# Kernel tuning notes

Hardware: AMD Instinct MI355X
Metric: run time of the kernel (lower is better)

## Reference

```python
import jax, jax.numpy as jnp
import numpy as np

B, T, N, DIN, HID, ED, K = 64, 12, 1024, 2, 64, 10, 2

def setup_inputs() -> dict:
    key = jax.random.key(0)
    ks = jax.random.split(key, 18)
    g = lambda i, shape, s=0.1: jax.random.normal(ks[i], shape, jnp.float32) * s
    return dict(
        x=g(0, (B, T, N, DIN), 1.0),
        node_embeddings=g(1, (N, ED), 1.0),
        # GCRN cell 0 (dim_in=DIN): gate -> 2*HID, update -> HID
        Wg0=g(2, (ED, K, DIN + HID, 2 * HID)), bg0=g(3, (ED, 2 * HID)),
        Wu0=g(4, (ED, K, DIN + HID, HID)),     bu0=g(5, (ED, HID)),
        # GCRN cell 1 (dim_in=HID)
        Wg1=g(6, (ED, K, 2 * HID, 2 * HID)),   bg1=g(7, (ED, 2 * HID)),
        Wu1=g(8, (ED, K, 2 * HID, HID)),       bu1=g(9, (ED, HID)),
        # RelatinoShipConv: pointwise Linear(input_dim -> rnn_units), torch [out,in]
        Wr=g(10, (HID, DIN)), br=g(11, (HID,)),
        # end_conv1: Linear(HID,HID, bias=False) (num_layers>1 branch)
        W1=g(12, (HID, HID)),
        # self.conv: Conv2d(horizon, horizon, (1, HID+1), bias=False), OIHW
        Wc=g(13, (T, T, 1, HID + 1)),
        # end_conv2: Conv2d(horizon, horizon, (1, HID), bias)
        W2=g(14, (T, T, 1, HID)), b2=g(15, (T,)),
        # end_conv3: Conv2d(horizon, horizon, (1, 2), dilation (1, HID), bias)
        W3=g(16, (T, T, 1, 2)), b3=g(17, (T,)),
    )

def _avwgcn(x, supports, E, Wp, bp):
    # x:[B,N,C], supports:[K,N,N], E:[N,ED] -> [B,N,O]  (AGCRN adaptive graph conv)
    xg = jnp.einsum('knm,bmc->bnkc', supports, x)
    W = jnp.einsum('ne,ekio->nkio', E, Wp)
    b = E @ bp
    return jnp.einsum('bnki,nkio->bno', xg, W) + b

def _cell(xt, h, supports, E, Wg, bg, Wu, bu):
    # GCRN GRU cell
    zr = jax.nn.sigmoid(_avwgcn(jnp.concatenate([xt, h], -1), supports, E, Wg, bg))
    z, r = jnp.split(zr, 2, -1)
    hc = jnp.tanh(_avwgcn(jnp.concatenate([xt, z * h], -1), supports, E, Wu, bu))
    return r * h + (1.0 - r) * hc

def _conv2d(x, w, b=None, rhs_dilation=(1, 1)):
    y = jax.lax.conv_general_dilated(x, w, (1, 1), 'VALID',
        rhs_dilation=rhs_dilation, dimension_numbers=('NCHW', 'OIHW', 'NCHW'))
    return y if b is None else y + b[None, :, None, None]

def _forward(x, E, Wg0, bg0, Wu0, bu0, Wg1, bg1, Wu1, bu1, Wr, br, W1, Wc, W2, b2, W3, b3):
    A = jax.nn.softmax(jax.nn.relu(E @ E.T), axis=1)
    supports = jnp.stack([jnp.eye(N, dtype=x.dtype), A], 0)  # [K,N,N]
    # GCRN encoder: python loop over 2 layers, lax.scan over the 12 timesteps
    cur = x
    for (Wg, bg, Wu, bu) in ((Wg0, bg0, Wu0, bu0), (Wg1, bg1, Wu1, bu1)):
        h0 = jnp.zeros((x.shape[0], N, HID), x.dtype)
        def step(h, xt):
            h = _cell(xt, h, supports, E, Wg, bg, Wu, bu)
            return h, h
        _, hs = jax.lax.scan(step, h0, jnp.swapaxes(cur, 0, 1))
        cur = jnp.swapaxes(hs, 0, 1)  # [B,T,N,HID]
    out = cur @ W1.T  # end_conv1 (Linear, no bias); dropout is identity in eval
    relation = x @ Wr.T + br  # [B,T,N,HID]
    # torch einsum 'btnc,knn->kbcnt' takes the DIAGONAL of supports over n
    rg = jnp.einsum('btnc,knn->kbcnt', relation, supports)
    rg = jnp.transpose(rg, (1, 4, 3, 2, 0)).reshape(x.shape[0], T, N, -1)  # [B,12,N,2*HID]
    rst = _conv2d(rg, Wc)  # [B,12,N,HID]
    out = _conv2d(jnp.concatenate([rst, out], -1), W2, b2)  # [B,12,N,HID+1]
    out = _conv2d(out, W3, b3, rhs_dilation=(1, HID))       # [B,12,N,1]
    return out

def reference(x, node_embeddings, Wg0, bg0, Wu0, bu0, Wg1, bg1, Wu1, bu1, Wr, br, W1, Wc, W2, b2, W3, b3):
    return _forward(x, node_embeddings, Wg0, bg0, Wu0, bu0, Wg1, bg1, Wu1, bu1, Wr, br, W1, Wc, W2, b2, W3, b3)
```

## Files before the change

### kernel.cpp

```cpp
#include <hip/hip_runtime.h>

typedef unsigned short u16;
typedef unsigned int   u32;


__device__ __forceinline__ float bf2f(u16 u){ return __uint_as_float(((u32)u)<<16); }
__device__ __forceinline__ u16 f2bf(float f){
  u32 u = __float_as_uint(f);
  return (u16)((u + 0x7fffu + ((u>>16)&1u)) >> 16);
}

__global__ __launch_bounds__(256) void k_A2(const float* __restrict__ E,
    float* __restrict__ A, float* __restrict__ At, float* __restrict__ diagA)
{
  __shared__ float EL[10][1024];
  __shared__ float row[1024];
  __shared__ float red[4];
  int n = blockIdx.x, tid = threadIdx.x;
  for (int idx=tid; idx<10240; idx+=256)
    EL[idx>>10][idx&1023] = E[(idx&1023)*10 + (idx>>10)];
  __syncthreads();
  float en[10];
#pragma unroll
  for (int e=0;e<10;++e) en[e] = EL[e][n];
  float lmax = -1e30f;
#pragma unroll
  for (int j=0;j<4;++j){
    int m = tid*4 + j;
    float d = 0.f;
#pragma unroll
    for (int e=0;e<10;++e) d = fmaf(en[e], EL[e][m], d);
    d = fmaxf(d, 0.f);
    row[m] = d; lmax = fmaxf(lmax, d);
  }
#pragma unroll
  for (int o=32;o>0;o>>=1) lmax = fmaxf(lmax, __shfl_xor(lmax, o));
  if ((tid&63)==0) red[tid>>6] = lmax;
  __syncthreads();
  float mx = fmaxf(fmaxf(red[0],red[1]), fmaxf(red[2],red[3]));
  __syncthreads();
  float lsum = 0.f;
#pragma unroll
  for (int j=0;j<4;++j){
    int m = tid*4 + j;
    float ex = expf(row[m] - mx);
    row[m] = ex; lsum += ex;
  }
#pragma unroll
  for (int o=32;o>0;o>>=1) lsum += __shfl_xor(lsum, o);
  if ((tid&63)==0) red[tid>>6] = lsum;
  __syncthreads();
  float inv = 1.f/(red[0]+red[1]+red[2]+red[3]);
#pragma unroll
  for (int j=0;j<4;++j){
    int m = tid*4 + j;
    float v = row[m]*inv;
    A[(size_t)n*1024 + m]  = v;
    At[(size_t)m*1024 + n] = v;
    if (m == n) diagA[n] = v;
  }
}

__global__ __launch_bounds__(64) void k_b3eff(
    const float* __restrict__ b2, const float* __restrict__ W3,
    const float* __restrict__ b3, float* __restrict__ b3eff)
{
  int o = threadIdx.x;
  if (o < 12){
    float a = b3[o];
    for (int i=0;i<12;++i)
      a += b2[i] * (W3[(o*12+i)*2] + W3[(o*12+i)*2+1]);
    b3eff[o] = a;
  }
}

__global__ __launch_bounds__(256) void k_Vpre(const float* __restrict__ W1,
    const float* __restrict__ W2, float* __restrict__ V)
{
  int idx = blockIdx.x*256 + threadIdx.x;
  if (idx >= 9216) return;
  int c = idx & 63, r = idx >> 6;
  int j = r % 12, i = r / 12;
  float a = 0.f;
  for (int o=0;o<64;++o)
    a = fmaf(W2[(i*12+j)*64+o], W1[o*64+c], a);
  V[idx] = a;
}

__global__ __launch_bounds__(256) void k_Gpre(const float* __restrict__ Wc,
    const float* __restrict__ W2, u16* __restrict__ G)
{
  int idx = blockIdx.x*256 + threadIdx.x;
  int u = idx & 127, r = idx >> 7;
  int ip = r % 12, i = r / 12;
  float a = 0.f;
  int wlo = u>64 ? u-64 : 0;
  int whi = u<63 ? u : 63;
  for (int j=0;j<12;++j){
    const float* w2r = W2 + (i*12+j)*64;
    const float* wcr = Wc + (j*12+ip)*65;
    for (int w=wlo; w<=whi; ++w)
      a = fmaf(w2r[w], wcr[u-w], a);
  }
  G[idx] = f2bf(a);
}

__global__ __launch_bounds__(256) void gemm7(const float* __restrict__ At,
    const float* __restrict__ X0, float* __restrict__ Y0,
    const float* __restrict__ X1, float* __restrict__ Y1)
{
  const float* X = blockIdx.z ? X1 : X0;
  float*       Y = blockIdx.z ? Y1 : Y0;
  int n0 = blockIdx.x * 128;
  long base = (long)blockIdx.y * 65536;
  __shared__ float Al[32*128];
  __shared__ float Xl[32*64];
  int tid = threadIdx.x;
  int tx = tid & 15, ty = tid >> 4;
  float acc[8][4];
#pragma unroll
  for (int r=0;r<8;++r){ acc[r][0]=0;acc[r][1]=0;acc[r][2]=0;acc[r][3]=0; }

  for (int m0=0; m0<1024; m0+=32){
#pragma unroll
    for (int i=0;i<4;++i){
      int fo = tid + i*256;
      int k = fo >> 5, nl4 = fo & 31;
      float4 v = *(const float4*)(At + (size_t)(m0+k)*1024 + n0 + nl4*4);
      *(float4*)(Al + fo*4) = v;
    }
#pragma unroll
    for (int i=0;i<2;++i){
      int fo = tid + i*256;
      float4 v = *(const float4*)(X + base + (long)m0*64 + fo*4);
      *(float4*)(Xl + fo*4) = v;
    }
    __syncthreads();
#pragma unroll
    for (int kk=0;kk<32;++kk){
      float4 xv = *(const float4*)(Xl + kk*64 + tx*4);
      float4 a0 = *(const float4*)(Al + kk*128 + ty*4);
      float4 a1 = *(const float4*)(Al + kk*128 + 64 + ty*4);
      float av[8] = {a0.x,a0.y,a0.z,a0.w,a1.x,a1.y,a1.z,a1.w};
      float xw[4] = {xv.x,xv.y,xv.z,xv.w};
#pragma unroll
      for (int r=0;r<8;++r)
#pragma unroll
        for (int c=0;c<4;++c) acc[r][c] = fmaf(av[r], xw[c], acc[r][c]);
    }
    __syncthreads();
  }
#pragma unroll
  for (int half=0; half<2; ++half)
#pragma unroll
    for (int i=0;i<4;++i){
      int row = n0 + half*64 + ty*4 + i;
      float4 v; v.x=acc[half*4+i][0]; v.y=acc[half*4+i][1];
      v.z=acc[half*4+i][2]; v.w=acc[half*4+i][3];
      *(float4*)&Y[base + (long)row*64 + tx*4] = v;
    }
}

__global__ __launch_bounds__(256) void gemm2x(const float* __restrict__ A,
    const float* __restrict__ x, float* __restrict__ Y)
{
  __shared__ float As[64][65];
  __shared__ float Xs[64][65];
  int n0 = blockIdx.x*64;
  int q0 = blockIdx.y*64;
  int tid = threadIdx.x, c = tid & 63, rq = tid >> 6;
  float acc[16];
#pragma unroll
  for (int j=0;j<16;++j) acc[j]=0.f;
  for (int m0=0; m0<1024; m0+=64){
#pragma unroll
    for (int j=0;j<16;++j){
      int idx = tid + j*256;
      int r = idx>>6, k = idx&63;
      As[r][k] = A[(size_t)(n0+r)*1024 + m0 + k];
      int qg = q0 + k;
      Xs[r][k] = x[(size_t)(qg>>1)*2048 + (size_t)(m0+r)*2 + (qg&1)];
    }
    __syncthreads();
    for (int k=0;k<64;++k){
      float xv = Xs[k][c];
#pragma unroll
      for (int j=0;j<16;++j) acc[j] = fmaf(As[rq+4*j][k], xv, acc[j]);
    }
    __syncthreads();
  }
#pragma unroll
  for (int j=0;j<16;++j)
    Y[(size_t)(n0+rq+4*j)*1536 + q0 + c] = acc[j];
}

template<int L>
__device__ __forceinline__ void gate_body(
    float* __restrict__ inp, float* __restrict__ Wl, float* __restrict__ En,
    const float* __restrict__ Wg, const float* __restrict__ bgp,
    const float* __restrict__ E,
    const float* __restrict__ xsrc, const float* __restrict__ Axt,
    const float* __restrict__ h, const float* __restrict__ Ah,
    float* __restrict__ zh, float* __restrict__ rb, int t, int first,
    int n, int b0, int tid)
{
  constexpr int IX  = (L==0)?2:64;
  constexpr int KI  = 2*(IX+64);
  constexpr int CH  = (L==0)?44:32;
  constexpr int NCH = KI/CH;
  constexpr int O   = 128;

  if (tid < 10) En[tid] = E[n*10 + tid];
  for (int idx=tid; idx<32*IX; idx+=256){
    int bl = idx/IX, i = idx - bl*IX; int b = b0+bl;
    inp[bl*KI + i] = (L==0)
      ? xsrc[(size_t)((b*12+t)*1024+n)*2 + i]
      : xsrc[((size_t)b<<16) + (size_t)n*64 + i];
  }
  for (int idx=tid; idx<2048; idx+=256){
    int bl = idx>>6, c = idx&63; int b = b0+bl;
    inp[bl*KI + IX + c] = first ? 0.f : h[((size_t)b<<16) + (size_t)n*64 + c];
  }
  for (int idx=tid; idx<32*IX; idx+=256){
    int bl = idx/IX, i = idx - bl*IX; int b = b0+bl;
    inp[bl*KI + IX+64+i] = (L==0)
      ? Axt[(size_t)n*1536 + (size_t)(b*12+t)*2 + i]
      : Axt[((size_t)b<<16) + (size_t)n*64 + i];
  }
  for (int idx=tid; idx<2048; idx+=256){
    int bl = idx>>6, c = idx&63; int b = b0+bl;
    inp[bl*KI + 2*IX+64+c] = first ? 0.f : Ah[((size_t)b<<16) + (size_t)n*64 + c];
  }
  __syncthreads();

  int bg = tid >> 5;
  int og = tid & 31;
  float acc[4][4];
#pragma unroll
  for (int d=0;d<4;++d){
    int o = og*4+d;
    float a = 0.f;
#pragma unroll
    for (int e=0;e<10;++e) a = fmaf(En[e], bgp[e*O+o], a);
#pragma unroll
    for (int bl=0;bl<4;++bl) acc[bl][d] = a;
  }

  for (int ch=0; ch<NCH; ++ch){
    for (int idx=tid; idx<CH*O; idx+=256){
      int i = idx>>7, o = idx&127;
      float a = 0.f;
#pragma unroll
      for (int e=0;e<10;++e)
        a = fmaf(En[e], Wg[((size_t)e*KI + ch*CH + i)*O + o], a);
      Wl[i*O + o] = a;
    }
    __syncthreads();
    float4 xq[4], wq[4];
#pragma unroll
    for (int bl=0;bl<4;++bl) xq[bl] = *(const float4*)&inp[(bg*4+bl)*KI + ch*CH];
#pragma unroll
    for (int ii=0;ii<4;++ii) wq[ii] = *(const float4*)&Wl[ii*O + og*4];
    for (int i=0; i<CH; i+=4){
      int i2 = (i+4<CH) ? i+4 : i;
      float4 xq2[4], wq2[4];
#pragma unroll
      for (int bl=0;bl<4;++bl) xq2[bl] = *(const float4*)&inp[(bg*4+bl)*KI + ch*CH + i2];
#pragma unroll
      for (int ii=0;ii<4;++ii) wq2[ii] = *(const float4*)&Wl[(i2+ii)*O + og*4];
      float xv[4][4], wv[4][4];
#pragma unroll
      for (int bl=0;bl<4;++bl){ xv[bl][0]=xq[bl].x; xv[bl][1]=xq[bl].y; xv[bl][2]=xq[bl].z; xv[bl][3]=xq[bl].w; }
#pragma unroll
      for (int ii=0;ii<4;++ii){ wv[ii][0]=wq[ii].x; wv[ii][1]=wq[ii].y; wv[ii][2]=wq[ii].z; wv[ii][3]=wq[ii].w; }
#pragma unroll
      for (int bl=0;bl<4;++bl)
#pragma unroll
        for (int d=0;d<4;++d)
#pragma unroll
          for (int ii=0;ii<4;++ii)
            acc[bl][d] = fmaf(xv[bl][ii], wv[ii][d], acc[bl][d]);
#pragma unroll
      for (int bl=0;bl<4;++bl) xq[bl]=xq2[bl];
#pragma unroll
      for (int ii=0;ii<4;++ii) wq[ii]=wq2[ii];
    }
    __syncthreads();
  }

#pragma unroll
  for (int bl=0;bl<4;++bl){
    int b = b0 + bg*4 + bl;
    size_t base = ((size_t)b<<16) + (size_t)n*64;
#pragma unroll
    for (int d=0;d<4;++d){
      int o = og*4 + d;
      float s = 1.f/(1.f+__expf(-acc[bl][d]));
      if (o < 64){
        if (!first) zh[base+o] = s * h[base+o];
      } else {
        rb[base+o-64] = s;
      }
    }
  }
}

__global__ __launch_bounds__(256) void k_gateB(int l_z0,
    const float* __restrict__ Wg0, const float* __restrict__ bg0,
    const float* __restrict__ Wg1, const float* __restrict__ bg1,
    const float* __restrict__ E,  const float* __restrict__ x,
    const float* __restrict__ Ax0T,
    const float* __restrict__ h0cur, const float* __restrict__ h1,
    const float* __restrict__ Axt1,  const float* __restrict__ AhZ1,
    float* __restrict__ zh0, float* __restrict__ rb0,
    float* __restrict__ zh1, float* __restrict__ rb1,
    int t0, int first0, int first1)
{
  __shared__ float smem[12288];
  __shared__ float En[10];
  int n = blockIdx.x, b0 = blockIdx.y*32, tid = threadIdx.x;
  int L = blockIdx.z ? 0 : l_z0;
  if (L == 1)
    gate_body<1>(smem, smem + 32*256, En, Wg1, bg1, E,
                 h0cur, Axt1, h1, AhZ1, zh1, rb1, 0, first1, n, b0, tid);
  else
    gate_body<0>(smem, smem + 32*132, En, Wg0, bg0, E,
                 x, Ax0T, h0cur, Axt1, zh0, rb0, t0, first0, n, b0, tid);
}

template<int L>
__device__ __forceinline__ void upd_body(
    float* __restrict__ inp, float* __restrict__ Wl, float* __restrict__ En,
    const float* __restrict__ Wu, const float* __restrict__ bup,
    const float* __restrict__ E,
    const float* __restrict__ xsrc, const float* __restrict__ Axt,
    const float* __restrict__ zh, const float* __restrict__ Azh,
    const float* __restrict__ rb,
    const float* __restrict__ hread, float* __restrict__ hwrite,
    const float* __restrict__ V, float* __restrict__ q1acc,
    int t, int tq, int first, int n, int b0, int tid)
{
  constexpr int IX  = (L==0)?2:64;
  constexpr int KI  = 2*(IX+64);
  constexpr int CH  = (L==0)?44:64;
  constexpr int NCH = KI/CH;
  constexpr int O   = 64;

  if (tid < 10) En[tid] = E[n*10 + tid];
  for (int idx=tid; idx<32*IX; idx+=256){
    int bl = idx/IX, i = idx - bl*IX; int b = b0+bl;
    inp[bl*KI + i] = (L==0)
      ? xsrc[(size_t)((b*12+t)*1024+n)*2 + i]
      : xsrc[((size_t)b<<16) + (size_t)n*64 + i];
  }
  for (int idx=tid; idx<2048; idx+=256){
    int bl = idx>>6, c = idx&63; int b = b0+bl;
    inp[bl*KI + IX + c] = first ? 0.f : zh[((size_t)b<<16) + (size_t)n*64 + c];
  }
  for (int idx=tid; idx<32*IX; idx+=256){
    int bl = idx/IX, i = idx - bl*IX; int b = b0+bl;
    inp[bl*KI + IX+64+i] = (L==0)
      ? Axt[(size_t)n*1536 + (size_t)(b*12+t)*2 + i]
      : Axt[((size_t)b<<16) + (size_t)n*64 + i];
  }
  for (int idx=tid; idx<2048; idx+=256){
    int bl = idx>>6, c = idx&63; int b = b0+bl;
    inp[bl*KI + 2*IX+64+c] = first ? 0.f : Azh[((size_t)b<<16) + (size_t)n*64 + c];
  }
  __syncthreads();

  int bg = tid >> 5;
  int og = tid & 31;
  float acc[4][2];
#pragma unroll
  for (int d=0;d<2;++d){
    int o = og*2+d;
    float a = 0.f;
#pragma unroll
    for (int e=0;e<10;++e) a = fmaf(En[e], bup[e*O+o], a);
#pragma unroll
    for (int bl=0;bl<4;++bl) acc[bl][d] = a;
  }

  for (int ch=0; ch<NCH; ++ch){
    for (int idx=tid; idx<CH*O; idx+=256){
      int i = idx>>6, o = idx&63;
      float a = 0.f;
#pragma unroll
      for (int e=0;e<10;++e)
        a = fmaf(En[e], Wu[((size_t)e*KI + ch*CH + i)*O + o], a);
      Wl[i*O + o] = a;
    }
    __syncthreads();
    float4 xq[4]; float2 wq[4];
#pragma unroll
    for (int bl=0;bl<4;++bl) xq[bl] = *(const float4*)&inp[(bg*4+bl)*KI + ch*CH];
#pragma unroll
    for (int ii=0;ii<4;++ii) wq[ii] = *(const float2*)&Wl[ii*O + og*2];
    for (int i=0; i<CH; i+=4){
      int i2 = (i+4<CH) ? i+4 : i;
      float4 xq2[4]; float2 wq2[4];
#pragma unroll
      for (int bl=0;bl<4;++bl) xq2[bl] = *(const float4*)&inp[(bg*4+bl)*KI + ch*CH + i2];
#pragma unroll
      for (int ii=0;ii<4;++ii) wq2[ii] = *(const float2*)&Wl[(i2+ii)*O + og*2];
      float xv[4][4], wv[4][2];
#pragma unroll
      for (int bl=0;bl<4;++bl){ xv[bl][0]=xq[bl].x; xv[bl][1]=xq[bl].y; xv[bl][2]=xq[bl].z; xv[bl][3]=xq[bl].w; }
#pragma unroll
      for (int ii=0;ii<4;++ii){ wv[ii][0]=wq[ii].x; wv[ii][1]=wq[ii].y; }
#pragma unroll
      for (int bl=0;bl<4;++bl)
#pragma unroll
        for (int d=0;d<2;++d)
#pragma unroll
          for (int ii=0;ii<4;++ii)
            acc[bl][d] = fmaf(xv[bl][ii], wv[ii][d], acc[bl][d]);
#pragma unroll
      for (int bl=0;bl<4;++bl) xq[bl]=xq2[bl];
#pragma unroll
      for (int ii=0;ii<4;++ii) wq[ii]=wq2[ii];
    }
    __syncthreads();
  }

  float* hnL = Wl;
  float* VL  = Wl + 2080;
#pragma unroll
  for (int bl=0;bl<4;++bl){
    int b = b0 + bg*4 + bl;
    size_t base = ((size_t)b<<16) + (size_t)n*64;
#pragma unroll
    for (int d=0;d<2;++d){
      int o = og*2 + d;
      float hc = tanhf(acc[bl][d]);
      float r  = rb[base+o];
      float h0v = first ? 0.f : hread[base+o];
      float hn = r*h0v + (1.f-r)*hc;
      hwrite[base+o] = hn;
      if (L==1) hnL[(bg*4+bl)*65 + o] = hn;
    }
  }
  if (L==1){
    for (int idx=tid; idx<768; idx+=256)
      VL[idx] = V[((idx>>6)*12+tq)*64 + (idx&63)];
    __syncthreads();
    for (int task=tid; task<384; task+=256){
      int bl = task & 31, i = task >> 5;
      const float* hv = hnL + bl*65;
      const float* vv = VL + i*64;
      float s = 0.f;
#pragma unroll 8
      for (int c=0;c<64;++c) s = fmaf(hv[c], vv[c], s);
      size_t qi = (((size_t)(b0+bl)<<10) + n)*12 + i;
      if (first) q1acc[qi] = s; else q1acc[qi] += s;
    }
  }
}

__global__ __launch_bounds__(256) void k_updB(int l_z0,
    const float* __restrict__ Wu0, const float* __restrict__ bu0,
    const float* __restrict__ Wu1, const float* __restrict__ bu1,
    const float* __restrict__ E,  const float* __restrict__ x,
    const float* __restrict__ Ax0T, const float* __restrict__ Axt1,
    const float* __restrict__ h0cur, float* __restrict__ h0new,
    float* __restrict__ h1,
    const float* __restrict__ zh0, const float* __restrict__ Azh0,
    const float* __restrict__ rb0,
    const float* __restrict__ zh1, const float* __restrict__ Azh1,
    const float* __restrict__ rb1,
    const float* __restrict__ V, float* __restrict__ q1acc,
    int t0, int t1, int first0, int first1)
{
  __shared__ float smem[12288];
  __shared__ float En[10];
  int n = blockIdx.x, b0 = blockIdx.y*32, tid = threadIdx.x;
  int L = blockIdx.z ? 0 : l_z0;
  if (L == 1)
    upd_body<1>(smem, smem + 32*256, En, Wu1, bu1, E,
                h0cur, Axt1, zh1, Azh1, rb1, h1, h1, V, q1acc,
                0, t1, first1, n, b0, tid);
  else
    upd_body<0>(smem, smem + 32*132, En, Wu0, bu0, E,
                x, Ax0T, zh0, Azh0, rb0, h0cur, h0new, nullptr, nullptr,
                t0, 0, first0, n, b0, tid);
}

__global__ __launch_bounds__(256) void k_q0G(
    const float* __restrict__ x, const float* __restrict__ diagA,
    const u16* __restrict__ G,
    const float* __restrict__ Wr, const float* __restrict__ br,
    float* __restrict__ q0buf)
{
  int n = blockIdx.x, tid = threadIdx.x;
  __shared__ u16  GL[18432];
  __shared__ float xsL[64][25];
  __shared__ float WrL[64][2];
  __shared__ float brL[64];

  for (int idx=tid; idx<18432; idx+=256) GL[idx] = G[idx];
  for (int idx=tid; idx<1536; idx+=256){
    int b = idx/24, r = idx - b*24;
    xsL[b][r] = x[(size_t)((b*12+(r>>1))*1024+n)*2 + (r&1)];
  }
  if (tid<128) WrL[tid>>1][tid&1] = Wr[tid];
  else if (tid<192) brL[tid-128] = br[tid-128];
  __syncthreads();

  float dA = diagA[n];
  int b = tid & 63, iq = tid >> 6;
  int i0 = iq*3;
  float q0a=0.f, q0b=0.f, q0c=0.f;
  for (int ip=0; ip<12; ++ip){
    float xa = xsL[b][ip*2], xb = xsL[b][ip*2+1];
    const u16* g0r = &GL[((i0+0)*12+ip)*128];
    const u16* g1r = &GL[((i0+1)*12+ip)*128];
    const u16* g2r = &GL[((i0+2)*12+ip)*128];
    for (int c=0;c<64;++c){
      float rel  = fmaf(xa, WrL[c][0], fmaf(xb, WrL[c][1], brL[c]));
      float relD = rel * dA;
      u32 g0 = *(const u32*)&g0r[2*c];
      u32 g1 = *(const u32*)&g1r[2*c];
      u32 g2 = *(const u32*)&g2r[2*c];
      q0a = fmaf(rel, bf2f((u16)g0), fmaf(relD, bf2f((u16)(g0>>16)), q0a));
      q0b = fmaf(rel, bf2f((u16)g1), fmaf(relD, bf2f((u16)(g1>>16)), q0b));
      q0c = fmaf(rel, bf2f((u16)g2), fmaf(relD, bf2f((u16)(g2>>16)), q0c));
    }
  }
  size_t qb = (((size_t)b<<10) + n)*12;
  q0buf[qb+i0]   = q0a;
  q0buf[qb+i0+1] = q0b;
  q0buf[qb+i0+2] = q0c;
}

__global__ __launch_bounds__(256) void k_head2(
    const float* __restrict__ q0buf, const float* __restrict__ q1acc,
    const float* __restrict__ W3, const float* __restrict__ b3eff,
    float* __restrict__ out)
{
  int n = blockIdx.x, tid = threadIdx.x;
  __shared__ float W3L[12][12][2];
  __shared__ float b3eL[12];
  __shared__ float q0L[64][12];
  __shared__ float q1L[64][12];

  if (tid < 12) b3eL[tid] = b3eff[tid];
  for (int idx=tid; idx<288; idx+=256){
    int o = idx/24, r = idx - o*24;
    W3L[o][r>>1][r&1] = W3[idx];
  }
  for (int idx=tid; idx<768; idx+=256){
    int b = idx/12, i = idx - (idx/12)*12;
    size_t base = (((size_t)b<<10) + n)*12 + i;
    q0L[b][i] = q0buf[base];
    q1L[b][i] = q1acc[base];
  }
  __syncthreads();

  for (int idx=tid; idx<768; idx+=256){
    int bb = idx/12, o = idx - (idx/12)*12;
    float a = b3eL[o];
#pragma unroll
    for (int i=0;i<12;++i)
      a += q0L[bb][i]*W3L[o][i][0] + q1L[bb][i]*W3L[o][i][1];
    out[(size_t)(bb*12+o)*1024 + n] = a;
  }
}

extern "C" void kernel_launch(void* const* d_in, const int* in_sizes, int n_in,
                              void* d_out, int out_size, void* d_ws, size_t ws_size,
                              hipStream_t stream)
{
  const float* x   = (const float*)d_in[0];
  const float* E   = (const float*)d_in[1];
  const float* Wg0 = (const float*)d_in[2];
  const float* bg0 = (const float*)d_in[3];
  const float* Wu0 = (const float*)d_in[4];
  const float* bu0 = (const float*)d_in[5];
  const float* Wg1 = (const float*)d_in[6];
  const float* bg1 = (const float*)d_in[7];
  const float* Wu1 = (const float*)d_in[8];
  const float* bu1 = (const float*)d_in[9];
  const float* Wr  = (const float*)d_in[10];
  const float* br  = (const float*)d_in[11];
  const float* W1  = (const float*)d_in[12];
  const float* Wc  = (const float*)d_in[13];
  const float* W2  = (const float*)d_in[14];
  const float* b2  = (const float*)d_in[15];
  const float* W3  = (const float*)d_in[16];
  const float* b3  = (const float*)d_in[17];

  char* ws = (char*)d_ws;
  size_t off = 0;
  auto alloc = [&](size_t bytes)->void*{
    void* p = ws + off; off += (bytes + 255) & ~(size_t)255; return p;
  };
  float* A     = (float*)alloc(1024ull*1024*4);
  float* At    = (float*)alloc(1024ull*1024*4);
  float* diagA = (float*)alloc(1024*4);
  float* Ax0T  = (float*)alloc(1024ull*1536*4);
  float* Axt1  = (float*)alloc(64ull*65536*4);
  float* AhZ1  = (float*)alloc(64ull*65536*4);
  float* Azh0  = (float*)alloc(64ull*65536*4);
  float* Azh1  = (float*)alloc(64ull*65536*4);
  float* zh0   = (float*)alloc(64ull*65536*4);
  float* zh1   = (float*)alloc(64ull*65536*4);
  float* rb0   = (float*)alloc(64ull*65536*4);
  float* rb1   = (float*)alloc(64ull*65536*4);
  float* h0a   = (float*)alloc(64ull*65536*4);
  float* h0b   = (float*)alloc(64ull*65536*4);
  float* h1    = (float*)alloc(64ull*65536*4);
  float* q1acc = (float*)alloc(64ull*1024*12*4);
  float* q0buf = (float*)alloc(64ull*1024*12*4);
  float* V     = (float*)alloc(12ull*12*64*4);
  u16*   G     = (u16*)alloc(12ull*12*128*2);
  float* b3eff = (float*)alloc(12*4);

  if (off > ws_size) return;

  k_A2<<<dim3(1024),256,0,stream>>>(E, A, At, diagA);
  k_b3eff<<<dim3(1),64,0,stream>>>(b2, W3, b3, b3eff);
  k_Vpre<<<dim3(36),256,0,stream>>>(W1, W2, V);
  k_Gpre<<<dim3(72),256,0,stream>>>(Wc, W2, G);
  gemm2x<<<dim3(16,24),256,0,stream>>>(A, x, Ax0T);
  k_q0G<<<dim3(1024),256,0,stream>>>(x, diagA, G, Wr, br, q0buf);

  k_gateB<<<dim3(1024,2,1),256,0,stream>>>(0, Wg0,bg0, Wg1,bg1, E, x, Ax0T,
      h0a, h1, Axt1, AhZ1, zh0, rb0, zh1, rb1, 0, 1, 0);
  k_updB<<<dim3(1024,2,1),256,0,stream>>>(0, Wu0,bu0, Wu1,bu1, E, x, Ax0T, Axt1,
      h0a, h0a, h1, zh0, Azh0, rb0, zh1, Azh1, rb1, V, q1acc, 0, 0, 1, 0);
  gemm7<<<dim3(8,64,1),256,0,stream>>>(At, h0a, Axt1, nullptr, nullptr);

  for (int k=0; k<12; ++k){
    int last   = (k == 11);
    int first1 = (k == 0);
    float* h0cur = (k&1) ? h0b : h0a;
    float* h0new = (k&1) ? h0a : h0b;

    k_gateB<<<dim3(1024,2, last?1:2),256,0,stream>>>(1, Wg0,bg0, Wg1,bg1,
        E, x, Ax0T, h0cur, h1, Axt1, AhZ1,
        zh0, rb0, zh1, rb1, k+1, 0, first1);

    if (first1)
      gemm7<<<dim3(8,64,1),256,0,stream>>>(At, zh0, Azh0, nullptr, nullptr);
    else if (last)
      gemm7<<<dim3(8,64,1),256,0,stream>>>(At, zh1, Azh1, nullptr, nullptr);
    else
      gemm7<<<dim3(8,64,2),256,0,stream>>>(At, zh1, Azh1, zh0, Azh0);

    k_updB<<<dim3(1024,2, last?1:2),256,0,stream>>>(1, Wu0,bu0, Wu1,bu1,
        E, x, Ax0T, Axt1, h0cur, h0new, h1,
        zh0, Azh0, rb0, zh1, Azh1, rb1, V, q1acc, k+1, k, 0, first1);

    if (!last)
      gemm7<<<dim3(8,64,2),256,0,stream>>>(At, h1, AhZ1, h0new, Axt1);
  }

  k_head2<<<dim3(1024),256,0,stream>>>(q0buf, q1acc, W3, b3eff, (float*)d_out);
}
```

Before: 10.36 ms.

## Precompute per-node combined weights once and double-buffer the adjacency GEMM

Adds a kernel that builds the per-node weight matrices E·Wp once for every gate and update cell and stores them in workspace. The gate and update kernels then copy those matrices instead of rebuilding them from the 10-term embedding sum on every timestep. This trades recomputation for a large extra memory footprint (about 300 MB) and more global reads each step. The adjacency GEMM is also rewritten with register-prefetched, double-buffered shared-memory tiles of depth 16, which removes one barrier per iteration.

```diff
diff --git a/kernel.cpp b/kernel.cpp
--- a/kernel.cpp
+++ b/kernel.cpp
@@ -105,7 +105,19 @@
   G[idx] = f2bf(a);
 }
 
-__global__ __launch_bounds__(256) void gemm7(const float* __restrict__ At,
+__global__ __launch_bounds__(256) void k_combF(const float* __restrict__ Wp,
+    const float* __restrict__ E, float* __restrict__ out, int plane)
+{
+  int n = blockIdx.x;
+  int j = blockIdx.y*256 + threadIdx.x;
+  if (j >= plane) return;
+  float a = 0.f;
+#pragma unroll
+  for (int e=0;e<10;++e) a = fmaf(E[n*10+e], Wp[(size_t)e*plane + j], a);
+  out[(size_t)n*plane + j] = a;
+}
+
+__global__ __launch_bounds__(256) void gemm8(const float* __restrict__ At,
     const float* __restrict__ X0, float* __restrict__ Y0,
     const float* __restrict__ X1, float* __restrict__ Y1)
 {
@@ -113,34 +125,37 @@
   float*       Y = blockIdx.z ? Y1 : Y0;
   int n0 = blockIdx.x * 128;
   long base = (long)blockIdx.y * 65536;
-  __shared__ float Al[32*128];
-  __shared__ float Xl[32*64];
+  __shared__ float Al[2][16*128];
+  __shared__ float Xl[2][16*64];
   int tid = threadIdx.x;
   int tx = tid & 15, ty = tid >> 4;
+  int ka0 = tid >> 5,  na = (tid & 31)*4;
+  int ka1 = ka0 + 8;
   float acc[8][4];
 #pragma unroll
   for (int r=0;r<8;++r){ acc[r][0]=0;acc[r][1]=0;acc[r][2]=0;acc[r][3]=0; }
 
-  for (int m0=0; m0<1024; m0+=32){
-#pragma unroll
-    for (int i=0;i<4;++i){
-      int fo = tid + i*256;
-      int k = fo >> 5, nl4 = fo & 31;
-      float4 v = *(const float4*)(At + (size_t)(m0+k)*1024 + n0 + nl4*4);
-      *(float4*)(Al + fo*4) = v;
-    }
-#pragma unroll
-    for (int i=0;i<2;++i){
-      int fo = tid + i*256;
-      float4 v = *(const float4*)(X + base + (long)m0*64 + fo*4);
-      *(float4*)(Xl + fo*4) = v;
-    }
+  float4 ra0 = *(const float4*)(At + (size_t)ka0*1024 + n0 + na);
+  float4 ra1 = *(const float4*)(At + (size_t)ka1*1024 + n0 + na);
+  float4 rx  = *(const float4*)(X + base + (long)tid*4);
+
+  for (int m0=0; m0<1024; m0+=16){
+    int cur = (m0>>4)&1;
+    *(float4*)(Al[cur] + tid*4)       = ra0;
+    *(float4*)(Al[cur] + (tid+256)*4) = ra1;
+    *(float4*)(Xl[cur] + tid*4)       = rx;
     __syncthreads();
-#pragma unroll
-    for (int kk=0;kk<32;++kk){
-      float4 xv = *(const float4*)(Xl + kk*64 + tx*4);
-      float4 a0 = *(const float4*)(Al + kk*128 + ty*4);
-      float4 a1 = *(const float4*)(Al + kk*128 + 64 + ty*4);
+    if (m0+16 < 1024){
+      int m1 = m0+16;
+      ra0 = *(const float4*)(At + (size_t)(m1+ka0)*1024 + n0 + na);
+      ra1 = *(const float4*)(At + (size_t)(m1+ka1)*1024 + n0 + na);
+      rx  = *(const float4*)(X + base + (long)m1*64 + (long)tid*4);
+    }
+#pragma unroll
+    for (int kk=0;kk<16;++kk){
+      float4 xv = *(const float4*)(Xl[cur] + kk*64 + tx*4);
+      float4 a0 = *(const float4*)(Al[cur] + kk*128 + ty*4);
+      float4 a1 = *(const float4*)(Al[cur] + kk*128 + 64 + ty*4);
       float av[8] = {a0.x,a0.y,a0.z,a0.w,a1.x,a1.y,a1.z,a1.w};
       float xw[4] = {xv.x,xv.y,xv.z,xv.w};
 #pragma unroll
@@ -148,7 +163,6 @@
 #pragma unroll
         for (int c=0;c<4;++c) acc[r][c] = fmaf(av[r], xw[c], acc[r][c]);
     }
-    __syncthreads();
   }
 #pragma unroll
   for (int half=0; half<2; ++half)
@@ -197,8 +211,8 @@
 template<int L>
 __device__ __forceinline__ void gate_body(
     float* __restrict__ inp, float* __restrict__ Wl, float* __restrict__ En,
-    const float* __restrict__ Wg, const float* __restrict__ bgp,
-    const float* __restrict__ E,
+    const float* __restrict__ Wg, const float* __restrict__ Wpre,
+    const float* __restrict__ bgp, const float* __restrict__ E,
     const float* __restrict__ xsrc, const float* __restrict__ Axt,
     const float* __restrict__ h, const float* __restrict__ Ah,
     float* __restrict__ zh, float* __restrict__ rb, int t, int first,
@@ -247,13 +261,18 @@
   }
 
   for (int ch=0; ch<NCH; ++ch){
-    for (int idx=tid; idx<CH*O; idx+=256){
-      int i = idx>>7, o = idx&127;
-      float a = 0.f;
-#pragma unroll
-      for (int e=0;e<10;++e)
-        a = fmaf(En[e], Wg[((size_t)e*KI + ch*CH + i)*O + o], a);
-      Wl[i*O + o] = a;
+    if (Wpre){
+      const float* src = Wpre + (size_t)n*(KI*O) + ch*CH*O;
+      for (int idx=tid; idx<CH*O; idx+=256) Wl[idx] = src[idx];
+    } else {
+      for (int idx=tid; idx<CH*O; idx+=256){
+        int i = idx>>7, o = idx&127;
+        float a = 0.f;
+#pragma unroll
+        for (int e=0;e<10;++e)
+          a = fmaf(En[e], Wg[((size_t)e*KI + ch*CH + i)*O + o], a);
+        Wl[i*O + o] = a;
+      }
     }
     __syncthreads();
     float4 xq[4], wq[4];
@@ -306,8 +325,10 @@
 }
 
 __global__ __launch_bounds__(256) void k_gateB(int l_z0,
-    const float* __restrict__ Wg0, const float* __restrict__ bg0,
-    const float* __restrict__ Wg1, const float* __restrict__ bg1,
+    const float* __restrict__ Wg0, const float* __restrict__ Wg0p,
+    const float* __restrict__ bg0,
+    const float* __restrict__ Wg1, const float* __restrict__ Wg1p,
+    const float* __restrict__ bg1,
     const float* __restrict__ E,  const float* __restrict__ x,
     const float* __restrict__ Ax0T,
     const float* __restrict__ h0cur, const float* __restrict__ h1,
@@ -321,18 +342,18 @@
   int n = blockIdx.x, b0 = blockIdx.y*32, tid = threadIdx.x;
   int L = blockIdx.z ? 0 : l_z0;
   if (L == 1)
-    gate_body<1>(smem, smem + 32*256, En, Wg1, bg1, E,
+    gate_body<1>(smem, smem + 32*256, En, Wg1, Wg1p, bg1, E,
                  h0cur, Axt1, h1, AhZ1, zh1, rb1, 0, first1, n, b0, tid);
   else
-    gate_body<0>(smem, smem + 32*132, En, Wg0, bg0, E,
+    gate_body<0>(smem, smem + 32*132, En, Wg0, Wg0p, bg0, E,
                  x, Ax0T, h0cur, Axt1, zh0, rb0, t0, first0, n, b0, tid);
 }
 
 template<int L>
 __device__ __forceinline__ void upd_body(
     float* __restrict__ inp, float* __restrict__ Wl, float* __restrict__ En,
-    const float* __restrict__ Wu, const float* __restrict__ bup,
-    const float* __restrict__ E,
+    const float* __restrict__ Wu, const float* __restrict__ Wpre,
+    const float* __restrict__ bup, const float* __restrict__ E,
     const float* __restrict__ xsrc, const float* __restrict__ Axt,
     const float* __restrict__ zh, const float* __restrict__ Azh,
     const float* __restrict__ rb,
@@ -383,13 +404,18 @@
   }
 
   for (int ch=0; ch<NCH; ++ch){
-    for (int idx=tid; idx<CH*O; idx+=256){
-      int i = idx>>6, o = idx&63;
-      float a = 0.f;
-#pragma unroll
-      for (int e=0;e<10;++e)
-        a = fmaf(En[e], Wu[((size_t)e*KI + ch*CH + i)*O + o], a);
-      Wl[i*O + o] = a;
+    if (Wpre){
+      const float* src = Wpre + (size_t)n*(KI*O) + ch*CH*O;
+      for (int idx=tid; idx<CH*O; idx+=256) Wl[idx] = src[idx];
+    } else {
+      for (int idx=tid; idx<CH*O; idx+=256){
+        int i = idx>>6, o = idx&63;
+        float a = 0.f;
+#pragma unroll
+        for (int e=0;e<10;++e)
+          a = fmaf(En[e], Wu[((size_t)e*KI + ch*CH + i)*O + o], a);
+        Wl[i*O + o] = a;
+      }
     }
     __syncthreads();
     float4 xq[4]; float2 wq[4];
@@ -459,8 +485,10 @@
 }
 
 __global__ __launch_bounds__(256) void k_updB(int l_z0,
-    const float* __restrict__ Wu0, const float* __restrict__ bu0,
-    const float* __restrict__ Wu1, const float* __restrict__ bu1,
+    const float* __restrict__ Wu0, const float* __restrict__ Wu0p,
+    const float* __restrict__ bu0,
+    const float* __restrict__ Wu1, const float* __restrict__ Wu1p,
+    const float* __restrict__ bu1,
     const float* __restrict__ E,  const float* __restrict__ x,
     const float* __restrict__ Ax0T, const float* __restrict__ Axt1,
     const float* __restrict__ h0cur, float* __restrict__ h0new,
@@ -477,11 +505,11 @@
   int n = blockIdx.x, b0 = blockIdx.y*32, tid = threadIdx.x;
   int L = blockIdx.z ? 0 : l_z0;
   if (L == 1)
-    upd_body<1>(smem, smem + 32*256, En, Wu1, bu1, E,
+    upd_body<1>(smem, smem + 32*256, En, Wu1, Wu1p, bu1, E,
                 h0cur, Axt1, zh1, Azh1, rb1, h1, h1, V, q1acc,
                 0, t1, first1, n, b0, tid);
   else
-    upd_body<0>(smem, smem + 32*132, En, Wu0, bu0, E,
+    upd_body<0>(smem, smem + 32*132, En, Wu0, Wu0p, bu0, E,
                 x, Ax0T, zh0, Azh0, rb0, h0cur, h0new, nullptr, nullptr,
                 t0, 0, first0, n, b0, tid);
 }
@@ -618,18 +646,33 @@
 
   if (off > ws_size) return;
 
+  auto tryAlloc = [&](size_t bytes)->float*{
+    size_t aligned = (bytes + 255) & ~(size_t)255;
+    if (off + aligned > ws_size) return (float*)nullptr;
+    void* p = ws + off; off += aligned; return (float*)p;
+  };
+  float* Wg1c = tryAlloc(1024ull*32768*4);
+  float* Wu1c = tryAlloc(1024ull*16384*4);
+  float* Wg0c = tryAlloc(1024ull*16896*4);
+  float* Wu0c = tryAlloc(1024ull*8448*4);
+
   k_A2<<<dim3(1024),256,0,stream>>>(E, A, At, diagA);
   k_b3eff<<<dim3(1),64,0,stream>>>(b2, W3, b3, b3eff);
   k_Vpre<<<dim3(36),256,0,stream>>>(W1, W2, V);
   k_Gpre<<<dim3(72),256,0,stream>>>(Wc, W2, G);
+  if (Wg1c) k_combF<<<dim3(1024,128),256,0,stream>>>(Wg1, E, Wg1c, 32768);
+  if (Wu1c) k_combF<<<dim3(1024, 64),256,0,stream>>>(Wu1, E, Wu1c, 16384);
+  if (Wg0c) k_combF<<<dim3(1024, 66),256,0,stream>>>(Wg0, E, Wg0c, 16896);
+  if (Wu0c) k_combF<<<dim3(1024, 33),256,0,stream>>>(Wu0, E, Wu0c,  8448);
   gemm2x<<<dim3(16,24),256,0,stream>>>(A, x, Ax0T);
   k_q0G<<<dim3(1024),256,0,stream>>>(x, diagA, G, Wr, br, q0buf);
 
-  k_gateB<<<dim3(1024,2,1),256,0,stream>>>(0, Wg0,bg0, Wg1,bg1, E, x, Ax0T,
-      h0a, h1, Axt1, AhZ1, zh0, rb0, zh1, rb1, 0, 1, 0);
-  k_updB<<<dim3(1024,2,1),256,0,stream>>>(0, Wu0,bu0, Wu1,bu1, E, x, Ax0T, Axt1,
-      h0a, h0a, h1, zh0, Azh0, rb0, zh1, Azh1, rb1, V, q1acc, 0, 0, 1, 0);
-  gemm7<<<dim3(8,64,1),256,0,stream>>>(At, h0a, Axt1, nullptr, nullptr);
+  k_gateB<<<dim3(1024,2,1),256,0,stream>>>(0, Wg0,Wg0c,bg0, Wg1,Wg1c,bg1,
+      E, x, Ax0T, h0a, h1, Axt1, AhZ1, zh0, rb0, zh1, rb1, 0, 1, 0);
+  k_updB<<<dim3(1024,2,1),256,0,stream>>>(0, Wu0,Wu0c,bu0, Wu1,Wu1c,bu1,
+      E, x, Ax0T, Axt1, h0a, h0a, h1, zh0, Azh0, rb0, zh1, Azh1, rb1,
+      V, q1acc, 0, 0, 1, 0);
+  gemm8<<<dim3(8,64,1),256,0,stream>>>(At, h0a, Axt1, nullptr, nullptr);
 
   for (int k=0; k<12; ++k){
     int last   = (k == 11);
@@ -637,23 +680,23 @@
     float* h0cur = (k&1) ? h0b : h0a;
     float* h0new = (k&1) ? h0a : h0b;
 
-    k_gateB<<<dim3(1024,2, last?1:2),256,0,stream>>>(1, Wg0,bg0, Wg1,bg1,
-        E, x, Ax0T, h0cur, h1, Axt1, AhZ1,
+    k_gateB<<<dim3(1024,2, last?1:2),256,0,stream>>>(1, Wg0,Wg0c,bg0,
+        Wg1,Wg1c,bg1, E, x, Ax0T, h0cur, h1, Axt1, AhZ1,
         zh0, rb0, zh1, rb1, k+1, 0, first1);
 
     if (first1)
-      gemm7<<<dim3(8,64,1),256,0,stream>>>(At, zh0, Azh0, nullptr, nullptr);
+      gemm8<<<dim3(8,64,1),256,0,stream>>>(At, zh0, Azh0, nullptr, nullptr);
     else if (last)
-      gemm7<<<dim3(8,64,1),256,0,stream>>>(At, zh1, Azh1, nullptr, nullptr);
+      gemm8<<<dim3(8,64,1),256,0,stream>>>(At, zh1, Azh1, nullptr, nullptr);
     else
-      gemm7<<<dim3(8,64,2),256,0,stream>>>(At, zh1, Azh1, zh0, Azh0);
-
-    k_updB<<<dim3(1024,2, last?1:2),256,0,stream>>>(1, Wu0,bu0, Wu1,bu1,
-        E, x, Ax0T, Axt1, h0cur, h0new, h1,
+      gemm8<<<dim3(8,64,2),256,0,stream>>>(At, zh1, Azh1, zh0, Azh0);
+
+    k_updB<<<dim3(1024,2, last?1:2),256,0,stream>>>(1, Wu0,Wu0c,bu0,
+        Wu1,Wu1c,bu1, E, x, Ax0T, Axt1, h0cur, h0new, h1,
         zh0, Azh0, rb0, zh1, Azh1, rb1, V, q1acc, k+1, k, 0, first1);
 
     if (!last)
-      gemm7<<<dim3(8,64,2),256,0,stream>>>(At, h1, AhZ1, h0new, Axt1);
+      gemm8<<<dim3(8,64,2),256,0,stream>>>(At, h1, AhZ1, h0new, Axt1);
   }
 
   k_head2<<<dim3(1024),256,0,stream>>>(q0buf, q1acc, W3, b3eff, (float*)d_out);
```

New measurement: 10.34 ms. No clear change (-0.2%).
